# Kernel tuning notes

Hardware: AMD Instinct MI355X
Metric: run time of the kernel (lower is better)

Reference implementation:

```python
import jax, jax.numpy as jnp
import numpy as np


def setup_inputs() -> dict:
    key = jax.random.key(0)
    k1, k2, k3, k4 = jax.random.split(key, 4)
    B, C, H, W = 4, 48, 512, 512
    T, ws = 3, 64
    # factor matrices (per TensorMultiplication_einsum, T summation terms)
    # init scale: 1/(init_temperature**(1/3) * sqrt(out_dim)) with init_temperature=1.0
    Ws = jax.random.normal(k2, (T, ws, ws), jnp.float32) / np.sqrt(ws)
    Hs = jax.random.normal(k3, (T, ws, ws), jnp.float32) / np.sqrt(ws)
    Cs = jax.random.normal(k4, (T, C, C), jnp.float32) / np.sqrt(C)
    x = jax.random.normal(k1, (B, C, H, W), jnp.float32)
    return {"x": x, "Ws": Ws, "Hs": Hs, "Cs": Cs, "window_size": ws}


def reference(x, Ws, Hs, Cs, window_size):
    """FeatureProcessingBlock forward:
      window_partition -> sum_t einsum('bchw,wW,hH,cC->bCHW') -> window_reverse.
    The window partition/reverse reshapes are fused into one einsum over the
    blocked view (p,q index the window grid; h,w index within-window pixels).
    """
    B, C, H, W = x.shape
    ws = window_size
    # (B, C, H//ws, ws, W//ws, ws)
    xb = x.reshape(B, C, H // ws, ws, W // ws, ws)
    # sum over T terms and contract w, h, c axes with their factor matrices
    out = jnp.einsum('bcphqw,twW,thH,tcC->bCpHqW', xb, Ws, Hs, Cs)
    return out.reshape(B, C, H, W)
```

## Files before the change

kernel.cpp:

```cpp
#include <hip/hip_runtime.h>
#include <hip/hip_bf16.h>


typedef __attribute__((ext_vector_type(8))) short short8;
typedef __attribute__((ext_vector_type(4))) short short4v;
typedef __attribute__((ext_vector_type(4))) float float4v;

#define SMEM_BYTES 145408

static __device__ __forceinline__ unsigned short f2bf(float f) {
  return __builtin_bit_cast(unsigned short, __float2bfloat16(f));
}

__global__ __launch_bounds__(1024)
void fpb7(const float* __restrict__ x, const float* __restrict__ Ws,
          const float* __restrict__ Hsm, const float* __restrict__ Cs,
          float* __restrict__ out) {
  extern __shared__ char smem[];
  char* Y1F = smem;
  char* Zb  = smem + 49152;
  char* Hf  = smem + 114688;
  char* Wf  = smem + 139264;

  int wid = (blockIdx.x & 7) * 128 + (blockIdx.x >> 3);
  int window = wid >> 2, tile = wid & 3;
  int b = window >> 6, p = (window >> 3) & 7, q = window & 7;
  int j0 = tile * 16;

  int tid = threadIdx.x, lane = tid & 63, wave = tid >> 6;
  int lq = lane >> 4, lc = lane & 15;

  int cA  = wave & 7, hh = wave >> 3;
  int mtB = wave & 3, cq = wave >> 2;

  if (wave < 6) {
    int t = wave >> 1, sv = wave & 1;
    short8 v;
    #pragma unroll
    for (int e = 0; e < 8; ++e)
      v[e] = (short)f2bf(Ws[t * 4096 + (32 * sv + 8 * lq + e) * 64 + j0 + lc]);
    *(short8*)(Wf + wave * 1024 + lane * 16) = v;
  }
  for (int j = wave; j < 24; j += 16) {
    int mt = j / 6, r6 = j - 6 * mt, t = r6 >> 1, sv = r6 & 1;
    short8 v;
    #pragma unroll
    for (int e = 0; e < 8; ++e)
      v[e] = (short)f2bf(Hsm[t * 4096 + (32 * sv + 8 * lq + e) * 64 + 16 * mt + lc]);
    *(short8*)(Hf + j * 1024 + lane * 16) = v;
  }

  float4v acc[3][4];
  #pragma unroll
  for (int m = 0; m < 3; ++m)
    #pragma unroll
    for (int i = 0; i < 4; ++i) acc[m][i] = float4v{0.f, 0.f, 0.f, 0.f};

  const float* sA = x + (((size_t)b * 48) * 512 + p * 64) * 512 + q * 64
                      + (size_t)cA * 262144 + (size_t)lc * 512 + 8 * lq;

  float4v fin[8];
  #pragma unroll
  for (int j2 = 0; j2 < 2; ++j2) {
    const float* r = sA + (size_t)(2 * hh + j2) * 8192;
    fin[4*j2+0] = *(const float4v*)(r);
    fin[4*j2+1] = *(const float4v*)(r + 4);
    fin[4*j2+2] = *(const float4v*)(r + 32);
    fin[4*j2+3] = *(const float4v*)(r + 36);
  }

  __syncthreads();

  for (int s = 0; s < 6; ++s) {
    {
      short8 af[4];
      #pragma unroll
      for (int j2 = 0; j2 < 2; ++j2) {
        short8 a0, a1;
        #pragma unroll
        for (int e2 = 0; e2 < 4; ++e2) {
          a0[e2]   = (short)f2bf(fin[4*j2+0][e2]);
          a0[4+e2] = (short)f2bf(fin[4*j2+1][e2]);
          a1[e2]   = (short)f2bf(fin[4*j2+2][e2]);
          a1[4+e2] = (short)f2bf(fin[4*j2+3][e2]);
        }
        af[2*j2] = a0; af[2*j2+1] = a1;
      }
      #pragma unroll
      for (int t = 0; t < 3; ++t) {
        short8 wf0 = *(const short8*)(Wf + (t * 2 + 0) * 1024 + lane * 16);
        short8 wf1 = *(const short8*)(Wf + (t * 2 + 1) * 1024 + lane * 16);
        #pragma unroll
        for (int j2 = 0; j2 < 2; ++j2) {
          float4v d = {0.f, 0.f, 0.f, 0.f};
          d = __builtin_amdgcn_mfma_f32_16x16x32_bf16(af[2*j2],   wf0, d, 0, 0, 0);
          d = __builtin_amdgcn_mfma_f32_16x16x32_bf16(af[2*j2+1], wf1, d, 0, 0, 0);
          int lqp = (2 * j2 + (lq >> 1)) & 3;
          short4v pv;
          pv[0] = (short)f2bf(d[0]); pv[1] = (short)f2bf(d[1]);
          pv[2] = (short)f2bf(d[2]); pv[3] = (short)f2bf(d[3]);
          *(short4v*)(Y1F + ((t * 8 + cA) * 2 + hh) * 1024
                          + (lqp * 16 + lc) * 16 + (lq & 1) * 8) = pv;
        }
      }
    }
    __syncthreads();

    {
      float craw[3][6];
      #pragma unroll
      for (int m = 0; m < 3; ++m)
        #pragma unroll
        for (int ch = 0; ch < 2; ++ch)
          #pragma unroll
          for (int t = 0; t < 3; ++t)
            craw[m][ch*3+t] =
                Cs[t * 2304 + (8 * s + 2 * lq + ch) * 48 + 16 * m + lc];

      unsigned long long w64[2][4];
      #pragma unroll
      for (int t = 0; t < 3; ++t) {
        short8 hf0 = *(const short8*)(Hf + (mtB * 6 + t * 2 + 0) * 1024 + lane * 16);
        short8 hf1 = *(const short8*)(Hf + (mtB * 6 + t * 2 + 1) * 1024 + lane * 16);
        #pragma unroll
        for (int cj = 0; cj < 2; ++cj) {
          const char* yb = Y1F + ((t * 8 + 2 * cq + cj) * 2) * 1024 + lane * 16;
          short8 y0 = *(const short8*)yb;
          short8 y1 = *(const short8*)(yb + 1024);
          float4v dd = {0.f, 0.f, 0.f, 0.f};
          dd = __builtin_amdgcn_mfma_f32_16x16x32_bf16(hf0, y0, dd, 0, 0, 0);
          dd = __builtin_amdgcn_mfma_f32_16x16x32_bf16(hf1, y1, dd, 0, 0, 0);
          #pragma unroll
          for (int r = 0; r < 4; ++r) {
            unsigned long long v = (unsigned long long)f2bf(dd[r]) << (16 * t);
            if (t == 0) w64[cj][r] = v; else w64[cj][r] |= v;
          }
        }
      }
      #pragma unroll
      for (int cj = 0; cj < 2; ++cj)
        #pragma unroll
        for (int r = 0; r < 4; ++r) {
          int px = (16 * mtB + 4 * lq + r) * 16 + lc;
          *(unsigned long long*)(Zb + cq * 16384 + px * 16 + cj * 8) = w64[cj][r];
        }

      short8 cf[3];
      #pragma unroll
      for (int m = 0; m < 3; ++m) {
        short8 v;
        v[0] = (short)f2bf(craw[m][0]); v[1] = (short)f2bf(craw[m][1]);
        v[2] = (short)f2bf(craw[m][2]); v[3] = 0;
        v[4] = (short)f2bf(craw[m][3]); v[5] = (short)f2bf(craw[m][4]);
        v[6] = (short)f2bf(craw[m][5]); v[7] = 0;
        cf[m] = v;
      }
      __syncthreads();

      if (s < 5) {
        #pragma unroll
        for (int j2 = 0; j2 < 2; ++j2) {
          const float* r = sA + (size_t)(s + 1) * 2097152 + (size_t)(2 * hh + j2) * 8192;
          fin[4*j2+0] = *(const float4v*)(r);
          fin[4*j2+1] = *(const float4v*)(r + 4);
          fin[4*j2+2] = *(const float4v*)(r + 32);
          fin[4*j2+3] = *(const float4v*)(r + 36);
        }
      }
      #pragma unroll
      for (int i = 0; i < 4; ++i) {
        int px = (wave + 16 * i) * 16 + lc;
        short8 zf = *(const short8*)(Zb + lq * 16384 + px * 16);
        acc[0][i] = __builtin_amdgcn_mfma_f32_16x16x32_bf16(cf[0], zf, acc[0][i], 0, 0, 0);
        acc[1][i] = __builtin_amdgcn_mfma_f32_16x16x32_bf16(cf[1], zf, acc[1][i], 0, 0, 0);
        acc[2][i] = __builtin_amdgcn_mfma_f32_16x16x32_bf16(cf[2], zf, acc[2][i], 0, 0, 0);
      }
    }
  }

  #pragma unroll
  for (int m = 0; m < 3; ++m)
    #pragma unroll
    for (int i = 0; i < 4; ++i) {
      int n = wave + 16 * i;
      #pragma unroll
      for (int r = 0; r < 4; ++r)
        out[(((size_t)(b * 48 + 16 * m + 4 * lq + r)) * 512 + p * 64 + n) * 512
            + q * 64 + j0 + lc] = acc[m][i][r];
    }
}

extern "C" void kernel_launch(void* const* d_in, const int* in_sizes, int n_in,
                              void* d_out, int out_size, void* d_ws, size_t ws_size,
                              hipStream_t stream) {
  (void)in_sizes; (void)n_in; (void)d_ws; (void)ws_size; (void)out_size;
  const float* x   = (const float*)d_in[0];
  const float* Ws  = (const float*)d_in[1];
  const float* Hsm = (const float*)d_in[2];
  const float* Cs  = (const float*)d_in[3];
  float* out = (float*)d_out;
  (void)hipFuncSetAttribute((const void*)fpb7,
                            hipFuncAttributeMaxDynamicSharedMemorySize, SMEM_BYTES);
  fpb7<<<dim3(1024), dim3(1024), SMEM_BYTES, stream>>>(x, Ws, Hsm, Cs, out);
}
```

Measured before the change: 177.3 us.

## Make blocks persistent over four windows and prefetch next window's input

The grid shrinks from 1024 to 256 blocks, one per CU, and each block now loops over four windows. The Ws/Hs fragments staged in shared memory are reused across windows, and the next window's first channel slice is prefetched during the last stage of the current one. This removes block launch overhead and the load bubble at the start of each block. The cost is fewer resident blocks, so there is less inter-block overlap, and the output stores now sit inside the window loop.

```diff
diff --git a/kernel.cpp b/kernel.cpp
--- a/kernel.cpp
+++ b/kernel.cpp
@@ -13,7 +13,7 @@
 }
 
 __global__ __launch_bounds__(1024)
-void fpb7(const float* __restrict__ x, const float* __restrict__ Ws,
+void fpb8(const float* __restrict__ x, const float* __restrict__ Ws,
           const float* __restrict__ Hsm, const float* __restrict__ Cs,
           float* __restrict__ out) {
   extern __shared__ char smem[];
@@ -22,9 +22,8 @@
   char* Hf  = smem + 114688;
   char* Wf  = smem + 139264;
 
-  int wid = (blockIdx.x & 7) * 128 + (blockIdx.x >> 3);
-  int window = wid >> 2, tile = wid & 3;
-  int b = window >> 6, p = (window >> 3) & 7, q = window & 7;
+  int xcd = blockIdx.x & 7, cu = blockIdx.x >> 3;
+  int tile = cu & 3, wslot = cu >> 2;
   int j0 = tile * 16;
 
   int tid = threadIdx.x, lane = tid & 63, wave = tid >> 6;
@@ -51,143 +50,160 @@
   }
 
   float4v acc[3][4];
-  #pragma unroll
-  for (int m = 0; m < 3; ++m)
-    #pragma unroll
-    for (int i = 0; i < 4; ++i) acc[m][i] = float4v{0.f, 0.f, 0.f, 0.f};
-
-  const float* sA = x + (((size_t)b * 48) * 512 + p * 64) * 512 + q * 64
-                      + (size_t)cA * 262144 + (size_t)lc * 512 + 8 * lq;
-
   float4v fin[8];
-  #pragma unroll
-  for (int j2 = 0; j2 < 2; ++j2) {
-    const float* r = sA + (size_t)(2 * hh + j2) * 8192;
-    fin[4*j2+0] = *(const float4v*)(r);
-    fin[4*j2+1] = *(const float4v*)(r + 4);
-    fin[4*j2+2] = *(const float4v*)(r + 32);
-    fin[4*j2+3] = *(const float4v*)(r + 36);
+
+  {
+    int w0 = xcd * 32 + wslot;
+    int b = w0 >> 6, p = (w0 >> 3) & 7, q = w0 & 7;
+    const float* s0 = x + (((size_t)b * 48) * 512 + p * 64) * 512 + q * 64
+                        + (size_t)cA * 262144 + (size_t)lc * 512 + 8 * lq;
+    #pragma unroll
+    for (int j2 = 0; j2 < 2; ++j2) {
+      const float* r = s0 + (size_t)(2 * hh + j2) * 8192;
+      fin[4*j2+0] = *(const float4v*)(r);
+      fin[4*j2+1] = *(const float4v*)(r + 4);
+      fin[4*j2+2] = *(const float4v*)(r + 32);
+      fin[4*j2+3] = *(const float4v*)(r + 36);
+    }
   }
 
   __syncthreads();
 
-  for (int s = 0; s < 6; ++s) {
-    {
-      short8 af[4];
+  #pragma unroll 1
+  for (int wit = 0; wit < 4; ++wit) {
+    int window = xcd * 32 + wslot + 8 * wit;
+    int b = window >> 6, p = (window >> 3) & 7, q = window & 7;
+    const float* sA = x + (((size_t)b * 48) * 512 + p * 64) * 512 + q * 64
+                        + (size_t)cA * 262144 + (size_t)lc * 512 + 8 * lq;
+    int wn = (wit < 3) ? (window + 8) : window;
+    int bn = wn >> 6, pn = (wn >> 3) & 7, qn = wn & 7;
+    const float* sAn = x + (((size_t)bn * 48) * 512 + pn * 64) * 512 + qn * 64
+                         + (size_t)cA * 262144 + (size_t)lc * 512 + 8 * lq;
+
+    #pragma unroll
+    for (int m = 0; m < 3; ++m)
       #pragma unroll
-      for (int j2 = 0; j2 < 2; ++j2) {
-        short8 a0, a1;
-        #pragma unroll
-        for (int e2 = 0; e2 < 4; ++e2) {
-          a0[e2]   = (short)f2bf(fin[4*j2+0][e2]);
-          a0[4+e2] = (short)f2bf(fin[4*j2+1][e2]);
-          a1[e2]   = (short)f2bf(fin[4*j2+2][e2]);
-          a1[4+e2] = (short)f2bf(fin[4*j2+3][e2]);
-        }
-        af[2*j2] = a0; af[2*j2+1] = a1;
+      for (int i = 0; i < 4; ++i) acc[m][i] = float4v{0.f, 0.f, 0.f, 0.f};
+
+    for (int s = 0; s < 6; ++s) {
+      {
+        short8 af[4];
+        #pragma unroll
+        for (int j2 = 0; j2 < 2; ++j2) {
+          short8 a0, a1;
+          #pragma unroll
+          for (int e2 = 0; e2 < 4; ++e2) {
+            a0[e2]   = (short)f2bf(fin[4*j2+0][e2]);
+            a0[4+e2] = (short)f2bf(fin[4*j2+1][e2]);
+            a1[e2]   = (short)f2bf(fin[4*j2+2][e2]);
+            a1[4+e2] = (short)f2bf(fin[4*j2+3][e2]);
+          }
+          af[2*j2] = a0; af[2*j2+1] = a1;
+        }
+        #pragma unroll
+        for (int t = 0; t < 3; ++t) {
+          short8 wf0 = *(const short8*)(Wf + (t * 2 + 0) * 1024 + lane * 16);
+          short8 wf1 = *(const short8*)(Wf + (t * 2 + 1) * 1024 + lane * 16);
+          #pragma unroll
+          for (int j2 = 0; j2 < 2; ++j2) {
+            float4v d = {0.f, 0.f, 0.f, 0.f};
+            d = __builtin_amdgcn_mfma_f32_16x16x32_bf16(af[2*j2],   wf0, d, 0, 0, 0);
+            d = __builtin_amdgcn_mfma_f32_16x16x32_bf16(af[2*j2+1], wf1, d, 0, 0, 0);
+            int lqp = (2 * j2 + (lq >> 1)) & 3;
+            short4v pv;
+            pv[0] = (short)f2bf(d[0]); pv[1] = (short)f2bf(d[1]);
+            pv[2] = (short)f2bf(d[2]); pv[3] = (short)f2bf(d[3]);
+            *(short4v*)(Y1F + ((t * 8 + cA) * 2 + hh) * 1024
+                            + (lqp * 16 + lc) * 16 + (lq & 1) * 8) = pv;
+          }
+        }
       }
-      #pragma unroll
-      for (int t = 0; t < 3; ++t) {
-        short8 wf0 = *(const short8*)(Wf + (t * 2 + 0) * 1024 + lane * 16);
-        short8 wf1 = *(const short8*)(Wf + (t * 2 + 1) * 1024 + lane * 16);
-        #pragma unroll
-        for (int j2 = 0; j2 < 2; ++j2) {
-          float4v d = {0.f, 0.f, 0.f, 0.f};
-          d = __builtin_amdgcn_mfma_f32_16x16x32_bf16(af[2*j2],   wf0, d, 0, 0, 0);
-          d = __builtin_amdgcn_mfma_f32_16x16x32_bf16(af[2*j2+1], wf1, d, 0, 0, 0);
-          int lqp = (2 * j2 + (lq >> 1)) & 3;
-          short4v pv;
-          pv[0] = (short)f2bf(d[0]); pv[1] = (short)f2bf(d[1]);
-          pv[2] = (short)f2bf(d[2]); pv[3] = (short)f2bf(d[3]);
-          *(short4v*)(Y1F + ((t * 8 + cA) * 2 + hh) * 1024
-                          + (lqp * 16 + lc) * 16 + (lq & 1) * 8) = pv;
+      __syncthreads();
+
+      {
+        float craw[3][6];
+        #pragma unroll
+        for (int m = 0; m < 3; ++m)
+          #pragma unroll
+          for (int ch = 0; ch < 2; ++ch)
+            #pragma unroll
+            for (int t = 0; t < 3; ++t)
+              craw[m][ch*3+t] =
+                  Cs[t * 2304 + (8 * s + 2 * lq + ch) * 48 + 16 * m + lc];
+
+        unsigned long long w64[2][4];
+        #pragma unroll
+        for (int t = 0; t < 3; ++t) {
+          short8 hf0 = *(const short8*)(Hf + (mtB * 6 + t * 2 + 0) * 1024 + lane * 16);
+          short8 hf1 = *(const short8*)(Hf + (mtB * 6 + t * 2 + 1) * 1024 + lane * 16);
+          #pragma unroll
+          for (int cj = 0; cj < 2; ++cj) {
+            const char* yb = Y1F + ((t * 8 + 2 * cq + cj) * 2) * 1024 + lane * 16;
+            short8 y0 = *(const short8*)yb;
+            short8 y1 = *(const short8*)(yb + 1024);
+            float4v dd = {0.f, 0.f, 0.f, 0.f};
+            dd = __builtin_amdgcn_mfma_f32_16x16x32_bf16(hf0, y0, dd, 0, 0, 0);
+            dd = __builtin_amdgcn_mfma_f32_16x16x32_bf16(hf1, y1, dd, 0, 0, 0);
+            #pragma unroll
+            for (int r = 0; r < 4; ++r) {
+              unsigned long long v = (unsigned long long)f2bf(dd[r]) << (16 * t);
+              if (t == 0) w64[cj][r] = v; else w64[cj][r] |= v;
+            }
+          }
+        }
+        #pragma unroll
+        for (int cj = 0; cj < 2; ++cj)
+          #pragma unroll
+          for (int r = 0; r < 4; ++r) {
+            int px = (16 * mtB + 4 * lq + r) * 16 + lc;
+            *(unsigned long long*)(Zb + cq * 16384 + px * 16 + cj * 8) = w64[cj][r];
+          }
+
+        short8 cf[3];
+        #pragma unroll
+        for (int m = 0; m < 3; ++m) {
+          short8 v;
+          v[0] = (short)f2bf(craw[m][0]); v[1] = (short)f2bf(craw[m][1]);
+          v[2] = (short)f2bf(craw[m][2]); v[3] = 0;
+          v[4] = (short)f2bf(craw[m][3]); v[5] = (short)f2bf(craw[m][4]);
+          v[6] = (short)f2bf(craw[m][5]); v[7] = 0;
+          cf[m] = v;
+        }
+        __syncthreads();
+
+        {
+          const float* pre = (s < 5) ? (sA + (size_t)(s + 1) * 2097152) : sAn;
+          #pragma unroll
+          for (int j2 = 0; j2 < 2; ++j2) {
+            const float* r = pre + (size_t)(2 * hh + j2) * 8192;
+            fin[4*j2+0] = *(const float4v*)(r);
+            fin[4*j2+1] = *(const float4v*)(r + 4);
+            fin[4*j2+2] = *(const float4v*)(r + 32);
+            fin[4*j2+3] = *(const float4v*)(r + 36);
+          }
+        }
+        #pragma unroll
+        for (int i = 0; i < 4; ++i) {
+          int px = (wave + 16 * i) * 16 + lc;
+          short8 zf = *(const short8*)(Zb + lq * 16384 + px * 16);
+          acc[0][i] = __builtin_amdgcn_mfma_f32_16x16x32_bf16(cf[0], zf, acc[0][i], 0, 0, 0);
+          acc[1][i] = __builtin_amdgcn_mfma_f32_16x16x32_bf16(cf[1], zf, acc[1][i], 0, 0, 0);
+          acc[2][i] = __builtin_amdgcn_mfma_f32_16x16x32_bf16(cf[2], zf, acc[2][i], 0, 0, 0);
         }
       }
     }
-    __syncthreads();
-
-    {
-      float craw[3][6];
-      #pragma unroll
-      for (int m = 0; m < 3; ++m)
-        #pragma unroll
-        for (int ch = 0; ch < 2; ++ch)
-          #pragma unroll
-          for (int t = 0; t < 3; ++t)
-            craw[m][ch*3+t] =
-                Cs[t * 2304 + (8 * s + 2 * lq + ch) * 48 + 16 * m + lc];
-
-      unsigned long long w64[2][4];
-      #pragma unroll
-      for (int t = 0; t < 3; ++t) {
-        short8 hf0 = *(const short8*)(Hf + (mtB * 6 + t * 2 + 0) * 1024 + lane * 16);
-        short8 hf1 = *(const short8*)(Hf + (mtB * 6 + t * 2 + 1) * 1024 + lane * 16);
-        #pragma unroll
-        for (int cj = 0; cj < 2; ++cj) {
-          const char* yb = Y1F + ((t * 8 + 2 * cq + cj) * 2) * 1024 + lane * 16;
-          short8 y0 = *(const short8*)yb;
-          short8 y1 = *(const short8*)(yb + 1024);
-          float4v dd = {0.f, 0.f, 0.f, 0.f};
-          dd = __builtin_amdgcn_mfma_f32_16x16x32_bf16(hf0, y0, dd, 0, 0, 0);
-          dd = __builtin_amdgcn_mfma_f32_16x16x32_bf16(hf1, y1, dd, 0, 0, 0);
-          #pragma unroll
-          for (int r = 0; r < 4; ++r) {
-            unsigned long long v = (unsigned long long)f2bf(dd[r]) << (16 * t);
-            if (t == 0) w64[cj][r] = v; else w64[cj][r] |= v;
-          }
-        }
-      }
-      #pragma unroll
-      for (int cj = 0; cj < 2; ++cj)
-        #pragma unroll
-        for (int r = 0; r < 4; ++r) {
-          int px = (16 * mtB + 4 * lq + r) * 16 + lc;
-          *(unsigned long long*)(Zb + cq * 16384 + px * 16 + cj * 8) = w64[cj][r];
-        }
-
-      short8 cf[3];
-      #pragma unroll
-      for (int m = 0; m < 3; ++m) {
-        short8 v;
-        v[0] = (short)f2bf(craw[m][0]); v[1] = (short)f2bf(craw[m][1]);
-        v[2] = (short)f2bf(craw[m][2]); v[3] = 0;
-        v[4] = (short)f2bf(craw[m][3]); v[5] = (short)f2bf(craw[m][4]);
-        v[6] = (short)f2bf(craw[m][5]); v[7] = 0;
-        cf[m] = v;
-      }
-      __syncthreads();
-
-      if (s < 5) {
-        #pragma unroll
-        for (int j2 = 0; j2 < 2; ++j2) {
-          const float* r = sA + (size_t)(s + 1) * 2097152 + (size_t)(2 * hh + j2) * 8192;
-          fin[4*j2+0] = *(const float4v*)(r);
-          fin[4*j2+1] = *(const float4v*)(r + 4);
-          fin[4*j2+2] = *(const float4v*)(r + 32);
-          fin[4*j2+3] = *(const float4v*)(r + 36);
-        }
-      }
+
+    #pragma unroll
+    for (int m = 0; m < 3; ++m)
       #pragma unroll
       for (int i = 0; i < 4; ++i) {
-        int px = (wave + 16 * i) * 16 + lc;
-        short8 zf = *(const short8*)(Zb + lq * 16384 + px * 16);
-        acc[0][i] = __builtin_amdgcn_mfma_f32_16x16x32_bf16(cf[0], zf, acc[0][i], 0, 0, 0);
-        acc[1][i] = __builtin_amdgcn_mfma_f32_16x16x32_bf16(cf[1], zf, acc[1][i], 0, 0, 0);
-        acc[2][i] = __builtin_amdgcn_mfma_f32_16x16x32_bf16(cf[2], zf, acc[2][i], 0, 0, 0);
+        int n = wave + 16 * i;
+        #pragma unroll
+        for (int r = 0; r < 4; ++r)
+          out[(((size_t)(b * 48 + 16 * m + 4 * lq + r)) * 512 + p * 64 + n) * 512
+              + q * 64 + j0 + lc] = acc[m][i][r];
       }
-    }
-  }
-
-  #pragma unroll
-  for (int m = 0; m < 3; ++m)
-    #pragma unroll
-    for (int i = 0; i < 4; ++i) {
-      int n = wave + 16 * i;
-      #pragma unroll
-      for (int r = 0; r < 4; ++r)
-        out[(((size_t)(b * 48 + 16 * m + 4 * lq + r)) * 512 + p * 64 + n) * 512
-            + q * 64 + j0 + lc] = acc[m][i][r];
-    }
+  }
 }
 
 extern "C" void kernel_launch(void* const* d_in, const int* in_sizes, int n_in,
@@ -199,7 +215,7 @@
   const float* Hsm = (const float*)d_in[2];
   const float* Cs  = (const float*)d_in[3];
   float* out = (float*)d_out;
-  (void)hipFuncSetAttribute((const void*)fpb7,
+  (void)hipFuncSetAttribute((const void*)fpb8,
                             hipFuncAttributeMaxDynamicSharedMemorySize, SMEM_BYTES);
-  fpb7<<<dim3(1024), dim3(1024), SMEM_BYTES, stream>>>(x, Ws, Hsm, Cs, out);
+  fpb8<<<dim3(256), dim3(1024), SMEM_BYTES, stream>>>(x, Ws, Hsm, Cs, out);
 }
```

Result: slower. 212.9 us (+20.0%).
